# Kernel tuning notes

Hardware: AMD Instinct MI355X
Metric: run time of the kernel (lower is better)

The kernel has to match this reference:

```python
import jax, jax.numpy as jnp
import numpy as np

WINDOW = 3
PAD = (WINDOW - 1) // 2  # reflect pad size


def setup_inputs() -> dict:
    key = jax.random.key(0)
    x = jax.random.normal(key, (8, 256, 256, 32), dtype=jnp.float32)
    return {"x": x}


def reference(x):
    # Reflect-pad spatially, then extract window x window patches.
    # Equivalent to TF depthwise_conv2d with a one-hot identity kernel:
    # output channel index = c * window^2 + i, where i = ki*window + kj.
    B, H, W, C = x.shape
    xp = jnp.pad(x, ((0, 0), (PAD, PAD), (PAD, PAD), (0, 0)), mode="reflect")
    # stack over the window^2 kernel taps (small fixed loop, not a data dim)
    patches = jnp.stack(
        [
            xp[:, (i // WINDOW):(i // WINDOW) + H, (i % WINDOW):(i % WINDOW) + W, :]
            for i in range(WINDOW * WINDOW)
        ],
        axis=-1,
    )  # [B, H, W, C, window^2]
    return patches.reshape(B, H, W, C * WINDOW * WINDOW)
```

## Files before the change

### kernel.cpp

```cpp
#include <hip/hip_runtime.h>


#define BB 8
#define HH 256
#define WW 256
#define CC 32
#define TAPS 9
#define OUTC (CC * TAPS)
#define TW 64
#define NTW (WW / TW)

__device__ __forceinline__ int refl(int i, int n) {
    return i < 0 ? -i : (i >= n ? 2 * n - 2 - i : i);
}

__global__ __launch_bounds__(256) void patch3x3_kernel(
    const float* __restrict__ x, float* __restrict__ out) {
    const int blk = blockIdx.x;
    const int wt = blk % NTW;
    const int h  = (blk / NTW) % HH;
    const int b  = blk / (NTW * HH);
    const int w0 = wt * TW;

    __shared__ float lds[3][TW + 2][CC];

    const int nload4 = 3 * (TW + 2) * (CC / 4);
    for (int idx = threadIdx.x; idx < nload4; idx += blockDim.x) {
        const int c4 = idx % (CC / 4);
        const int wl = (idx / (CC / 4)) % (TW + 2);
        const int r  = idx / ((CC / 4) * (TW + 2));
        const int gh = refl(h + r - 1, HH);
        const int gw = refl(w0 + wl - 1, WW);
        const float4* src =
            (const float4*)(x + (((b * HH + gh) * WW + gw) * CC)) + c4;
        ((float4*)&lds[r][wl][0])[c4] = *src;
    }
    __syncthreads();

    float4* outp = (float4*)(out + (size_t)(((b * HH + h) * WW + w0)) * OUTC);
    const int nout4 = TW * (OUTC / 4);
    for (int idx = threadIdx.x; idx < nout4; idx += blockDim.x) {
        const int j = idx % (OUTC / 4);
        const int p = idx / (OUTC / 4);
        const int f = 4 * j;
        float4 v;
#pragma unroll
        for (int k = 0; k < 4; ++k) {
            const int fk = f + k;
            const int c  = fk / TAPS;
            const int i  = fk % TAPS;
            const int ki = i / 3;
            const int kj = i % 3;
            ((float*)&v)[k] = lds[ki][p + kj][c];
        }
        outp[idx] = v;
    }
}

extern "C" void kernel_launch(void* const* d_in, const int* in_sizes, int n_in,
                              void* d_out, int out_size, void* d_ws, size_t ws_size,
                              hipStream_t stream) {
    const float* x = (const float*)d_in[0];
    float* out = (float*)d_out;
    const int nblocks = BB * HH * NTW;
    patch3x3_kernel<<<nblocks, 256, 0, stream>>>(x, out);
}
```

Measured before the change: 627.0 us.

## Gather 3x3 patches into registers and stage output tile through LDS

Each thread now owns one pixel and four channels. It loads the nine neighbouring float4 vectors from LDS into registers, permutes them into the channel-major tap order, and writes the result to an output LDS tile. The tile is then streamed to global memory with fully coalesced float4 stores. The per-element scalar LDS reads and div/mod index arithmetic of the old path go away. The tile width is halved so the output staging buffer fits in shared memory, at the cost of more blocks and more halo overhead.

```diff
diff --git a/kernel.cpp b/kernel.cpp
--- a/kernel.cpp
+++ b/kernel.cpp
@@ -7,25 +7,27 @@
 #define CC 32
 #define TAPS 9
 #define OUTC (CC * TAPS)
-#define TW 64
+#define TW 32
 #define NTW (WW / TW)
 
 __device__ __forceinline__ int refl(int i, int n) {
     return i < 0 ? -i : (i >= n ? 2 * n - 2 - i : i);
 }
 
-__global__ __launch_bounds__(256) void patch3x3_kernel(
+__global__ __launch_bounds__(256) void patch3x3_v2(
     const float* __restrict__ x, float* __restrict__ out) {
     const int blk = blockIdx.x;
     const int wt = blk % NTW;
     const int h  = (blk / NTW) % HH;
     const int b  = blk / (NTW * HH);
     const int w0 = wt * TW;
+    const int t  = threadIdx.x;
 
-    __shared__ float lds[3][TW + 2][CC];
+    __shared__ float in_lds[3][TW + 2][CC];
+    __shared__ float out_lds[TW][OUTC];
 
     const int nload4 = 3 * (TW + 2) * (CC / 4);
-    for (int idx = threadIdx.x; idx < nload4; idx += blockDim.x) {
+    for (int idx = t; idx < nload4; idx += 256) {
         const int c4 = idx % (CC / 4);
         const int wl = (idx / (CC / 4)) % (TW + 2);
         const int r  = idx / ((CC / 4) * (TW + 2));
@@ -33,27 +35,43 @@
         const int gw = refl(w0 + wl - 1, WW);
         const float4* src =
             (const float4*)(x + (((b * HH + gh) * WW + gw) * CC)) + c4;
-        ((float4*)&lds[r][wl][0])[c4] = *src;
+        *((float4*)&in_lds[r][wl][0] + c4) = *src;
     }
     __syncthreads();
 
-    float4* outp = (float4*)(out + (size_t)(((b * HH + h) * WW + w0)) * OUTC);
-    const int nout4 = TW * (OUTC / 4);
-    for (int idx = threadIdx.x; idx < nout4; idx += blockDim.x) {
-        const int j = idx % (OUTC / 4);
-        const int p = idx / (OUTC / 4);
-        const int f = 4 * j;
-        float4 v;
+    {
+        const int p  = t >> 3;
+        const int cg = t & 7;
+        float4 q[3][3];
 #pragma unroll
-        for (int k = 0; k < 4; ++k) {
-            const int fk = f + k;
-            const int c  = fk / TAPS;
-            const int i  = fk % TAPS;
-            const int ki = i / 3;
-            const int kj = i % 3;
-            ((float*)&v)[k] = lds[ki][p + kj][c];
+        for (int ki = 0; ki < 3; ++ki)
+#pragma unroll
+            for (int kj = 0; kj < 3; ++kj)
+                q[ki][kj] = *(const float4*)&in_lds[ki][p + kj][cg * 4];
+
+#pragma unroll
+        for (int m = 0; m < 9; ++m) {
+            float4 v;
+#pragma unroll
+            for (int k = 0; k < 4; ++k) {
+                const int f  = 4 * m + k;
+                const int cl = f / 9;
+                const int i  = f % 9;
+                const int ki = i / 3;
+                const int kj = i % 3;
+                ((float*)&v)[k] = ((const float*)&q[ki][kj])[cl];
+            }
+            *(float4*)&out_lds[p][cg * 36 + 4 * m] = v;
         }
-        outp[idx] = v;
+    }
+    __syncthreads();
+
+    float4* outp = (float4*)(out + (size_t)((b * HH + h) * WW + w0) * OUTC);
+    const float4* src4 = (const float4*)&out_lds[0][0];
+#pragma unroll
+    for (int it = 0; it < (TW * OUTC / 4) / 256; ++it) {
+        const int idx = t + 256 * it;
+        outp[idx] = src4[idx];
     }
 }
 
@@ -63,5 +81,5 @@
     const float* x = (const float*)d_in[0];
     float* out = (float*)d_out;
     const int nblocks = BB * HH * NTW;
-    patch3x3_kernel<<<nblocks, 256, 0, stream>>>(x, out);
+    patch3x3_v2<<<nblocks, 256, 0, stream>>>(x, out);
 }
```

Result: slower. 639.6 us (+2.0%).
